# Optimization experiments

Measured on AMD Instinct MI355X. Metric: run time of the kernel, lower is better.

## Reference

```python
import jax, jax.numpy as jnp
import numpy as np

B, SQ, SK, H, A = 4, 512, 512, 256, 128

def setup_inputs() -> dict:
    key = jax.random.key(0)
    ks = jax.random.split(key, 8)
    s = 1.0 / np.sqrt(H)
    sa = 1.0 / np.sqrt(A)
    return {
        "Q": jax.random.normal(ks[0], (B, SQ, H), dtype=jnp.float32),
        "K": jax.random.normal(ks[1], (B, SK, H), dtype=jnp.float32),
        "V": jax.random.normal(ks[2], (B, SK, H), dtype=jnp.float32),
        "W_q": jax.random.uniform(ks[3], (H, A), jnp.float32, -s, s),
        "W_k": jax.random.uniform(ks[4], (H, A), jnp.float32, -s, s),
        "v": jax.random.uniform(ks[5], (A,), jnp.float32, -sa, sa),
        "W_o": jax.random.uniform(ks[6], (H, H), jnp.float32, -s, s),
        "b_o": jax.random.uniform(ks[7], (H,), jnp.float32, -s, s),
    }

def reference(Q, K, V, W_q, W_k, v, W_o, b_o):
    # Q: (B, Sq, H), K/V: (B, Sk, H)
    Qt = Q @ W_q                      # (B, Sq, A)
    Kt = K @ W_k                      # (B, Sk, A)
    additive = jnp.tanh(Qt[:, :, None, :] + Kt[:, None, :, :])  # (B, Sq, Sk, A)
    scores = jnp.einsum('bqka,a->bqk', additive, v)             # (B, Sq, Sk)
    weights = jax.nn.softmax(scores, axis=-1)                   # (B, Sq, Sk)
    out = jnp.einsum('bqk,bkh->bqh', weights, V)                 # (B, Sq, H)
    out = out @ W_o + b_o
    return (out, weights)
```

## Files before the change

### kernel.cpp

```cpp
#include <hip/hip_runtime.h>
#include <math.h>

#define BB 4
#define SQL 512
#define SKL 512
#define HH 256
#define AA 128

#define PRESCALE 2.8853900817779268f

__device__ inline void fma4(float4& a, float s, const float4& b) {
    a.x = fmaf(s, b.x, a.x); a.y = fmaf(s, b.y, a.y);
    a.z = fmaf(s, b.z, a.z); a.w = fmaf(s, b.w, a.w);
}

__global__ __launch_bounds__(256, 4) void prep_kernel(
    const float* __restrict__ Q, const float* __restrict__ K,
    const float* __restrict__ V,
    const float* __restrict__ Wq, const float* __restrict__ Wk,
    const float* __restrict__ Wo,
    float* __restrict__ Qt, float* __restrict__ Kt, float* __restrict__ VW)
{
    __shared__ float rows[8 * HH];
    __shared__ float wl[64 * 128];
    int tid = threadIdx.x;
    int bid = blockIdx.x;

    const float* X; const float* W; float* Y;
    int ldW, ldY, col0, r0; float scale;
    if (bid < 256)      { X=Q; W=Wq; Y=Qt; ldW=AA; ldY=AA; col0=0; r0=bid*8;        scale=PRESCALE; }
    else if (bid < 512) { X=K; W=Wk; Y=Kt; ldW=AA; ldY=AA; col0=0; r0=(bid-256)*8;  scale=PRESCALE; }
    else { int b2=bid-512; X=V; W=Wo; Y=VW; ldW=HH; ldY=HH; col0=(b2&1)*128; r0=(b2>>1)*8; scale=1.0f; }

    {
        const float4* Xv = (const float4*)(X + (size_t)r0 * HH);
        float4* rv = (float4*)rows;
        rv[tid]       = Xv[tid];
        rv[tid + 256] = Xv[tid + 256];
    }

    int r  = tid >> 5;
    int c4 = tid & 31;
    float4 acc = {0.f, 0.f, 0.f, 0.f};

    for (int ch = 0; ch < 4; ++ch) {
        __syncthreads();
        {
            const float* Wbase = W + (size_t)(ch * 64) * ldW + col0;
            float4* wv = (float4*)wl;
            #pragma unroll
            for (int it = 0; it < 8; ++it) {
                int l = tid + it * 256;
                wv[l] = *(const float4*)(Wbase + (size_t)(l >> 5) * ldW + ((l & 31) << 2));
            }
        }
        __syncthreads();
        const float* rrow = rows + r * HH + ch * 64;
        #pragma unroll 4
        for (int h4 = 0; h4 < 16; ++h4) {
            float4 rv = *(const float4*)(rrow + h4 * 4);
            const float* wbase = wl + (h4 * 4) * 128 + (c4 << 2);
            float4 w0 = *(const float4*)(wbase);
            float4 w1 = *(const float4*)(wbase + 128);
            float4 w2 = *(const float4*)(wbase + 256);
            float4 w3 = *(const float4*)(wbase + 384);
            fma4(acc, rv.x, w0); fma4(acc, rv.y, w1);
            fma4(acc, rv.z, w2); fma4(acc, rv.w, w3);
        }
    }
    acc.x *= scale; acc.y *= scale; acc.z *= scale; acc.w *= scale;
    *(float4*)(Y + (size_t)(r0 + r) * ldY + col0 + (c4 << 2)) = acc;
}

__global__ __launch_bounds__(256, 4) void score_kernel(
    const float* __restrict__ Qt, const float* __restrict__ Kt,
    const float* __restrict__ v,  const float* __restrict__ VW,
    const float* __restrict__ bo,
    float* __restrict__ weights,  float* __restrict__ out)
{
    __shared__ float kt_lds[32 * 129];
    __shared__ float score[2][SKL];
    __shared__ float part[2][8][32];
    __shared__ float pout[4][2][HH];
    __shared__ float vv[AA];

    int tid = threadIdx.x;
    int b  = blockIdx.x >> 8;
    int q0 = (blockIdx.x & 255) << 1;
    int kl = tid & 31;
    int ag = tid >> 5;

    if (tid < AA) vv[tid] = v[tid];

    float qreg0[16], qreg1[16], v2reg[16];
    {
        const float* vp = v + ag * 16;
        const float* qp0 = Qt + (size_t)(b * SQL + q0)     * AA + ag * 16;
        const float* qp1 = Qt + (size_t)(b * SQL + q0 + 1) * AA + ag * 16;
        #pragma unroll
        for (int j = 0; j < 16; ++j) {
            v2reg[j] = 2.0f * vp[j];
            qreg0[j] = qp0[j];
            qreg1[j] = qp1[j];
        }
    }
    __syncthreads();
    float S_all = 0.f;
    #pragma unroll
    for (int a = 0; a < AA; ++a) S_all += vv[a];

    for (int c = 0; c < 16; ++c) {
        {
            const float4* Kv = (const float4*)(Kt + (size_t)(b * SKL + c * 32) * AA);
            #pragma unroll
            for (int it = 0; it < 4; ++it) {
                int l = tid + it * 256;
                int rr = l >> 5, cc = (l & 31) << 2;
                float4 val = Kv[l];
                float* dst = kt_lds + rr * 129 + cc;
                dst[0] = val.x; dst[1] = val.y; dst[2] = val.z; dst[3] = val.w;
            }
        }
        __syncthreads();

        float p0 = 0.f, p1 = 0.f;
        const float* kp = kt_lds + kl * 129 + ag * 16;
        #pragma unroll
        for (int j = 0; j < 16; ++j) {
            float kv = kp[j];
            float x0 = qreg0[j] + kv;
            float x1 = qreg1[j] + kv;
            float e0 = __builtin_amdgcn_exp2f(x0);
            float e1 = __builtin_amdgcn_exp2f(x1);
            float r0 = __builtin_amdgcn_rcpf(e0 + 1.0f);
            float r1 = __builtin_amdgcn_rcpf(e1 + 1.0f);
            p0 = fmaf(v2reg[j], r0, p0);
            p1 = fmaf(v2reg[j], r1, p1);
        }
        part[0][ag][kl] = p0;
        part[1][ag][kl] = p1;
        __syncthreads();

        if (tid < 64) {
            int qi = tid >> 5, kk = tid & 31;
            float s = 0.f;
            #pragma unroll
            for (int g = 0; g < 8; ++g) s += part[qi][g][kk];
            score[qi][c * 32 + kk] = S_all - s;
        }
    }
    __syncthreads();

    int wave = tid >> 6, lane = tid & 63;
    if (wave < 2) {
        int qi = wave;
        float m = -1e30f;
        for (int k = lane; k < SKL; k += 64) m = fmaxf(m, score[qi][k]);
        #pragma unroll
        for (int off = 32; off; off >>= 1) m = fmaxf(m, __shfl_xor(m, off));
        float s = 0.f;
        for (int k = lane; k < SKL; k += 64) {
            float e = __builtin_amdgcn_exp2f((score[qi][k] - m) * 1.44269504f);
            score[qi][k] = e;
            s += e;
        }
        #pragma unroll
        for (int off = 32; off; off >>= 1) s += __shfl_xor(s, off);
        float rinv = 1.0f / s;
        size_t rowoff = (size_t)(b * SQL + q0 + qi) * SKL;
        for (int k = lane; k < SKL; k += 64) {
            float wv2 = score[qi][k] * rinv;
            score[qi][k] = wv2;
            weights[rowoff + k] = wv2;
        }
    }
    __syncthreads();

    {
        const float4* VWb = (const float4*)(VW + (size_t)b * SKL * HH);
        float4 a0 = {0,0,0,0}, a1 = {0,0,0,0};
        int kbase = wave * 128;
        #pragma unroll 4
        for (int k = 0; k < 128; ++k) {
            int kk = kbase + k;
            float4 vw4 = VWb[kk * (HH / 4) + lane];
            float w0 = score[0][kk];
            float w1 = score[1][kk];
            fma4(a0, w0, vw4);
            fma4(a1, w1, vw4);
        }
        *(float4*)&pout[wave][0][lane << 2] = a0;
        *(float4*)&pout[wave][1][lane << 2] = a1;
    }
    __syncthreads();
    {
        int h = tid;
        float bias = bo[h];
        #pragma unroll
        for (int qi = 0; qi < 2; ++qi) {
            float s = bias + pout[0][qi][h] + pout[1][qi][h]
                           + pout[2][qi][h] + pout[3][qi][h];
            out[(size_t)(b * SQL + q0 + qi) * HH + h] = s;
        }
    }
}

extern "C" void kernel_launch(void* const* d_in, const int* in_sizes, int n_in,
                              void* d_out, int out_size, void* d_ws, size_t ws_size,
                              hipStream_t stream)
{
    const float* Q  = (const float*)d_in[0];
    const float* K  = (const float*)d_in[1];
    const float* V  = (const float*)d_in[2];
    const float* Wq = (const float*)d_in[3];
    const float* Wk = (const float*)d_in[4];
    const float* v  = (const float*)d_in[5];
    const float* Wo = (const float*)d_in[6];
    const float* bo = (const float*)d_in[7];

    float* out     = (float*)d_out;
    float* weights = out + (size_t)BB * SQL * HH;

    float* Qt = (float*)d_ws;
    float* Kt = Qt + (size_t)BB * SQL * AA;
    float* VW = Kt + (size_t)BB * SKL * AA;

    prep_kernel <<<1024, 256, 0, stream>>>(Q, K, V, Wq, Wk, Wo, Qt, Kt, VW);
    score_kernel<<<1024, 256, 0, stream>>>(Qt, Kt, v, VW, bo, weights, out);
}
```

Measured before the change: 137.5 us.

## Drop LDS staging of Kt in score kernel; double rows per prep block

The score kernel no longer stages Kt tiles in shared memory with per-chunk barriers. Each thread now loads its 16-element Kt slice straight from global memory, and partial sums are reduced with wave shuffles instead of an LDS partial-sum array. S_all is likewise computed with shuffles. The prep kernel now computes 16 rows per block with two accumulators, halving the grid and reusing each W tile from LDS twice. The trade-off is fewer barriers and less LDS traffic against more direct, less coalesced global/L2 loads of Kt and higher register use.

```diff
diff --git a/kernel.cpp b/kernel.cpp
--- a/kernel.cpp
+++ b/kernel.cpp
@@ -14,34 +14,36 @@
     a.z = fmaf(s, b.z, a.z); a.w = fmaf(s, b.w, a.w);
 }
 
-__global__ __launch_bounds__(256, 4) void prep_kernel(
+__global__ __launch_bounds__(256) void prep_kernel(
     const float* __restrict__ Q, const float* __restrict__ K,
     const float* __restrict__ V,
     const float* __restrict__ Wq, const float* __restrict__ Wk,
     const float* __restrict__ Wo,
     float* __restrict__ Qt, float* __restrict__ Kt, float* __restrict__ VW)
 {
-    __shared__ float rows[8 * HH];
+    __shared__ float rows[16 * HH];
     __shared__ float wl[64 * 128];
     int tid = threadIdx.x;
     int bid = blockIdx.x;
 
     const float* X; const float* W; float* Y;
     int ldW, ldY, col0, r0; float scale;
-    if (bid < 256)      { X=Q; W=Wq; Y=Qt; ldW=AA; ldY=AA; col0=0; r0=bid*8;        scale=PRESCALE; }
-    else if (bid < 512) { X=K; W=Wk; Y=Kt; ldW=AA; ldY=AA; col0=0; r0=(bid-256)*8;  scale=PRESCALE; }
-    else { int b2=bid-512; X=V; W=Wo; Y=VW; ldW=HH; ldY=HH; col0=(b2&1)*128; r0=(b2>>1)*8; scale=1.0f; }
+    if (bid < 128)      { X=Q; W=Wq; Y=Qt; ldW=AA; ldY=AA; col0=0; r0=bid*16;       scale=PRESCALE; }
+    else if (bid < 256) { X=K; W=Wk; Y=Kt; ldW=AA; ldY=AA; col0=0; r0=(bid-128)*16; scale=PRESCALE; }
+    else { int b2=bid-256; X=V; W=Wo; Y=VW; ldW=HH; ldY=HH; col0=(b2&1)*128; r0=(b2>>1)*16; scale=1.0f; }
 
     {
         const float4* Xv = (const float4*)(X + (size_t)r0 * HH);
         float4* rv = (float4*)rows;
         rv[tid]       = Xv[tid];
         rv[tid + 256] = Xv[tid + 256];
+        rv[tid + 512] = Xv[tid + 512];
+        rv[tid + 768] = Xv[tid + 768];
     }
 
     int r  = tid >> 5;
     int c4 = tid & 31;
-    float4 acc = {0.f, 0.f, 0.f, 0.f};
+    float4 accA = {0.f,0.f,0.f,0.f}, accB = {0.f,0.f,0.f,0.f};
 
     for (int ch = 0; ch < 4; ++ch) {
         __syncthreads();
@@ -55,79 +57,85 @@
             }
         }
         __syncthreads();
-        const float* rrow = rows + r * HH + ch * 64;
+        const float* rrowA = rows + r * HH + ch * 64;
+        const float* rrowB = rows + (r + 8) * HH + ch * 64;
         #pragma unroll 4
         for (int h4 = 0; h4 < 16; ++h4) {
-            float4 rv = *(const float4*)(rrow + h4 * 4);
+            float4 ra = *(const float4*)(rrowA + h4 * 4);
+            float4 rb = *(const float4*)(rrowB + h4 * 4);
             const float* wbase = wl + (h4 * 4) * 128 + (c4 << 2);
             float4 w0 = *(const float4*)(wbase);
             float4 w1 = *(const float4*)(wbase + 128);
             float4 w2 = *(const float4*)(wbase + 256);
             float4 w3 = *(const float4*)(wbase + 384);
-            fma4(acc, rv.x, w0); fma4(acc, rv.y, w1);
-            fma4(acc, rv.z, w2); fma4(acc, rv.w, w3);
-        }
-    }
-    acc.x *= scale; acc.y *= scale; acc.z *= scale; acc.w *= scale;
-    *(float4*)(Y + (size_t)(r0 + r) * ldY + col0 + (c4 << 2)) = acc;
-}
-
-__global__ __launch_bounds__(256, 4) void score_kernel(
+            fma4(accA, ra.x, w0); fma4(accA, ra.y, w1);
+            fma4(accA, ra.z, w2); fma4(accA, ra.w, w3);
+            fma4(accB, rb.x, w0); fma4(accB, rb.y, w1);
+            fma4(accB, rb.z, w2); fma4(accB, rb.w, w3);
+        }
+    }
+    accA.x *= scale; accA.y *= scale; accA.z *= scale; accA.w *= scale;
+    accB.x *= scale; accB.y *= scale; accB.z *= scale; accB.w *= scale;
+    *(float4*)(Y + (size_t)(r0 + r)     * ldY + col0 + (c4 << 2)) = accA;
+    *(float4*)(Y + (size_t)(r0 + r + 8) * ldY + col0 + (c4 << 2)) = accB;
+}
+
+__global__ __launch_bounds__(256) void score_kernel(
     const float* __restrict__ Qt, const float* __restrict__ Kt,
     const float* __restrict__ v,  const float* __restrict__ VW,
     const float* __restrict__ bo,
     float* __restrict__ weights,  float* __restrict__ out)
 {
-    __shared__ float kt_lds[32 * 129];
     __shared__ float score[2][SKL];
-    __shared__ float part[2][8][32];
     __shared__ float pout[4][2][HH];
-    __shared__ float vv[AA];
 
     int tid = threadIdx.x;
     int b  = blockIdx.x >> 8;
     int q0 = (blockIdx.x & 255) << 1;
-    int kl = tid & 31;
-    int ag = tid >> 5;
-
-    if (tid < AA) vv[tid] = v[tid];
+    int ag = tid & 7;
+    int kl = tid >> 3;
 
     float qreg0[16], qreg1[16], v2reg[16];
     {
-        const float* vp = v + ag * 16;
-        const float* qp0 = Qt + (size_t)(b * SQL + q0)     * AA + ag * 16;
-        const float* qp1 = Qt + (size_t)(b * SQL + q0 + 1) * AA + ag * 16;
+        const float4* vp  = (const float4*)(v + ag * 16);
+        const float4* qp0 = (const float4*)(Qt + (size_t)(b * SQL + q0)     * AA + ag * 16);
+        const float4* qp1 = (const float4*)(Qt + (size_t)(b * SQL + q0 + 1) * AA + ag * 16);
+        #pragma unroll
+        for (int j4 = 0; j4 < 4; ++j4) {
+            float4 vv4 = vp[j4];
+            *(float4*)&qreg0[j4 * 4] = qp0[j4];
+            *(float4*)&qreg1[j4 * 4] = qp1[j4];
+            v2reg[j4 * 4 + 0] = 2.0f * vv4.x;
+            v2reg[j4 * 4 + 1] = 2.0f * vv4.y;
+            v2reg[j4 * 4 + 2] = 2.0f * vv4.z;
+            v2reg[j4 * 4 + 3] = 2.0f * vv4.w;
+        }
+    }
+
+    float S_all;
+    {
+        float ls = 0.f;
+        #pragma unroll
+        for (int j = 0; j < 16; ++j) ls += v2reg[j];
+        ls += __shfl_xor(ls, 1);
+        ls += __shfl_xor(ls, 2);
+        ls += __shfl_xor(ls, 4);
+        S_all = 0.5f * ls;
+    }
+
+    for (int c = 0; c < 16; ++c) {
+        int k = c * 32 + kl;
+        const float4* kt4 = (const float4*)(Kt + (size_t)(b * SKL + k) * AA + ag * 16);
+        float kt[16];
+        *(float4*)&kt[0]  = kt4[0];
+        *(float4*)&kt[4]  = kt4[1];
+        *(float4*)&kt[8]  = kt4[2];
+        *(float4*)&kt[12] = kt4[3];
+
+        float p0 = 0.f, p1 = 0.f;
         #pragma unroll
         for (int j = 0; j < 16; ++j) {
-            v2reg[j] = 2.0f * vp[j];
-            qreg0[j] = qp0[j];
-            qreg1[j] = qp1[j];
-        }
-    }
-    __syncthreads();
-    float S_all = 0.f;
-    #pragma unroll
-    for (int a = 0; a < AA; ++a) S_all += vv[a];
-
-    for (int c = 0; c < 16; ++c) {
-        {
-            const float4* Kv = (const float4*)(Kt + (size_t)(b * SKL + c * 32) * AA);
-            #pragma unroll
-            for (int it = 0; it < 4; ++it) {
-                int l = tid + it * 256;
-                int rr = l >> 5, cc = (l & 31) << 2;
-                float4 val = Kv[l];
-                float* dst = kt_lds + rr * 129 + cc;
-                dst[0] = val.x; dst[1] = val.y; dst[2] = val.z; dst[3] = val.w;
-            }
-        }
-        __syncthreads();
-
-        float p0 = 0.f, p1 = 0.f;
-        const float* kp = kt_lds + kl * 129 + ag * 16;
-        #pragma unroll
-        for (int j = 0; j < 16; ++j) {
-            float kv = kp[j];
+            float kv = kt[j];
             float x0 = qreg0[j] + kv;
             float x1 = qreg1[j] + kv;
             float e0 = __builtin_amdgcn_exp2f(x0);
@@ -137,16 +145,12 @@
             p0 = fmaf(v2reg[j], r0, p0);
             p1 = fmaf(v2reg[j], r1, p1);
         }
-        part[0][ag][kl] = p0;
-        part[1][ag][kl] = p1;
-        __syncthreads();
-
-        if (tid < 64) {
-            int qi = tid >> 5, kk = tid & 31;
-            float s = 0.f;
-            #pragma unroll
-            for (int g = 0; g < 8; ++g) s += part[qi][g][kk];
-            score[qi][c * 32 + kk] = S_all - s;
+        p0 += __shfl_xor(p0, 1); p1 += __shfl_xor(p1, 1);
+        p0 += __shfl_xor(p0, 2); p1 += __shfl_xor(p1, 2);
+        p0 += __shfl_xor(p0, 4); p1 += __shfl_xor(p1, 4);
+        if (ag == 0) {
+            score[0][k] = S_all - p0;
+            score[1][k] = S_all - p1;
         }
     }
     __syncthreads();
@@ -225,6 +229,6 @@
     float* Kt = Qt + (size_t)BB * SQL * AA;
     float* VW = Kt + (size_t)BB * SKL * AA;
 
-    prep_kernel <<<1024, 256, 0, stream>>>(Q, K, V, Wq, Wk, Wo, Qt, Kt, VW);
+    prep_kernel <<<512, 256, 0, stream>>>(Q, K, V, Wq, Wk, Wo, Qt, Kt, VW);
     score_kernel<<<1024, 256, 0, stream>>>(Qt, Kt, v, VW, bo, weights, out);
 }
```

Measured after the change: 129.8 us. 5.6% less time.
